# Kernel tuning notes

Hardware: AMD Instinct MI355X
Metric: run time of the kernel (lower is better)

The kernel has to match this reference:

```python
import jax, jax.numpy as jnp
import numpy as np

DECAY = 0.99
EPS = 1e-5
COMMITMENT_COST = 0.25
K = 8192   # n_embeddings
D = 256    # embedding_dim


def setup_inputs() -> dict:
    key = jax.random.key(0)
    k_z, k_w = jax.random.split(key)
    z = jax.random.normal(k_z, (16, 1024, D), dtype=jnp.float32)
    # torch init: uniform(-1/K, 1/K)
    weight = jax.random.uniform(k_w, (K, D), dtype=jnp.float32,
                                minval=-1.0 / K, maxval=1.0 / K)
    ema_cluster_size = jnp.zeros((K,), dtype=jnp.float32)
    ema_w = weight  # ema_w initialized to codebook weights
    return {"z": z, "weight": weight,
            "ema_cluster_size": ema_cluster_size, "ema_w": ema_w}


def reference(z, weight, ema_cluster_size, ema_w):
    flat = z.reshape(-1, D)                                   # [N, D]
    dist = (jnp.sum(flat * flat, axis=1, keepdims=True)
            - 2.0 * flat @ weight.T
            + jnp.sum(weight * weight, axis=1))
    idx = jnp.argmin(dist, axis=1)                            # [N]
    quantized = weight[idx].reshape(z.shape)                  # gather

    # EMA codebook update (training path)
    counts = jax.ops.segment_sum(jnp.ones_like(idx, dtype=jnp.float32),
                                 idx, num_segments=K)          # [K]
    dw = jax.ops.segment_sum(flat, idx, num_segments=K)       # [K, D]
    new_cluster_size = DECAY * ema_cluster_size + (1.0 - DECAY) * counts
    new_ema_w = DECAY * ema_w + (1.0 - DECAY) * dw
    n = jnp.sum(new_cluster_size)
    cluster_size = (new_cluster_size + EPS) / (n + K * EPS) * n
    new_weight = new_ema_w / cluster_size[:, None]

    # straight-through estimator + losses
    quantized_st = z + jax.lax.stop_gradient(quantized - z)
    codebook_loss = jnp.mean((jax.lax.stop_gradient(quantized) - z) ** 2)
    commitment_loss = jnp.mean((quantized - jax.lax.stop_gradient(z)) ** 2)
    loss = codebook_loss + COMMITMENT_COST * commitment_loss

    encoding_indices = idx.reshape(z.shape[:-1])
    return (quantized_st, loss, encoding_indices,
            new_weight, new_cluster_size, new_ema_w)
```

## Files before the change

### kernel.cpp

```cpp
#include <hip/hip_runtime.h>


#define NTOK 16384
#define KC   8192
#define DD   256

#define OFF_Q    0
#define OFF_LOSS 4194304
#define OFF_IDX  4194305
#define OFF_W    4210689
#define OFF_CS   6307841
#define OFF_EMA  6316033

#define DECAY_F  0.99f
#define OMD_F    0.01f
#define EPS_F    1e-5f
#define KEPS_F   0.08192f

typedef __attribute__((address_space(3))) unsigned int lds_u;
typedef const __attribute__((address_space(1))) unsigned int glob_u;

__global__ __launch_bounds__(256) void k_tr(const float* __restrict__ in,
                                            float* __restrict__ outT,
                                            int R, int C) {
    __shared__ float s[32][33];
    const int tx = threadIdx.x & 31, ty = threadIdx.x >> 5;
    const int c0 = blockIdx.x * 32, r0 = blockIdx.y * 32;
    #pragma unroll
    for (int i = 0; i < 4; ++i)
        s[ty + i * 8][tx] = in[(size_t)(r0 + ty + i * 8) * C + c0 + tx];
    __syncthreads();
    #pragma unroll
    for (int i = 0; i < 4; ++i)
        outT[(size_t)(c0 + ty + i * 8) * R + r0 + tx] = s[tx][ty + i * 8];
}

__global__ __launch_bounds__(256) void k_rownorm(const float* __restrict__ a,
                                                 float* __restrict__ outn) {
    const int wave = threadIdx.x >> 6, lane = threadIdx.x & 63;
    const int row  = blockIdx.x * 16 + wave * 4 + (lane >> 4);
    const int p    = lane & 15;
    const int h    = p >> 3, j = p & 7;
    const float* base = a + row * DD + h * 128 + j;
    float v = base[0];
    float r = __fmul_rn(v, v);
    #pragma unroll
    for (int t = 1; t < 16; ++t) {
        v = base[8 * t];
        r = __fadd_rn(r, __fmul_rn(v, v));
    }
    r = __fadd_rn(r, __shfl_xor(r, 1));
    r = __fadd_rn(r, __shfl_xor(r, 2));
    r = __fadd_rn(r, __shfl_xor(r, 4));
    r = __fadd_rn(r, __shfl_xor(r, 8));
    if (p == 0) outn[row] = r;
}

__global__ __launch_bounds__(256, 4) void k_argmin(
        const float* __restrict__ zT, const float* __restrict__ wT,
        const float* __restrict__ x2v, const float* __restrict__ w2v,
        float* __restrict__ vbuf, int* __restrict__ kbuf) {
    __shared__ float Zs[32][128];
    __shared__ float Ws[32][128];

    const int tid   = threadIdx.x;
    const int split = blockIdx.x & 7;
    const int rb    = blockIdx.x >> 3;
    const int n0    = rb * 128;
    const int cbase = split * 1024;
    const int tx4   = (tid & 15) * 4;
    const int ty4   = (tid >> 4) * 4;
    const int l     = tid & 63;
    const int wv    = tid >> 6;
    const int lcol  = (l & 31) * 4;
    const int lrow2 = l >> 5;

    float bestv[8];
    int   bestk[8];
    #pragma unroll
    for (int i = 0; i < 8; ++i) { bestv[i] = 1e30f; bestk[i] = 0; }

    for (int kt = 0; kt < 8; ++kt) {
        const int c0 = cbase + kt * 128;
        float acc[8][8] = {};
        for (int dt = 0; dt < 8; ++dt) {
            const int d0 = dt * 32;
            __syncthreads();
            #pragma unroll
            for (int q = 0; q < 4; ++q) {
                const int m  = wv * 4 + q;
                const int dd = m * 2 + lrow2;
                const float* gz = zT + (size_t)(d0 + dd) * NTOK + n0 + lcol;
                const float* gw = wT + (size_t)(d0 + dd) * KC   + c0 + lcol;
                __builtin_amdgcn_global_load_lds(
                    (glob_u*)gz, (lds_u*)((char*)&Zs[0][0] + m * 1024 + l * 16),
                    16, 0, 0);
                __builtin_amdgcn_global_load_lds(
                    (glob_u*)gw, (lds_u*)((char*)&Ws[0][0] + m * 1024 + l * 16),
                    16, 0, 0);
            }
            __syncthreads();
            #pragma unroll 8
            for (int dd = 0; dd < 32; ++dd) {
                const float4 a0 = *(const float4*)&Zs[dd][ty4];
                const float4 a1 = *(const float4*)&Zs[dd][64 + ty4];
                const float4 b0 = *(const float4*)&Ws[dd][tx4];
                const float4 b1 = *(const float4*)&Ws[dd][64 + tx4];
                const float av[8] = {a0.x, a0.y, a0.z, a0.w, a1.x, a1.y, a1.z, a1.w};
                const float bw[8] = {b0.x, b0.y, b0.z, b0.w, b1.x, b1.y, b1.z, b1.w};
                #pragma unroll
                for (int i = 0; i < 8; ++i)
                    #pragma unroll
                    for (int j = 0; j < 8; ++j)
                        acc[i][j] = __fmaf_rn(av[i], bw[j], acc[i][j]);
            }
        }
        #pragma unroll
        for (int j = 0; j < 8; ++j) {
            const int   code = c0 + ((j < 4) ? (tx4 + j) : (64 + tx4 + j - 4));
            const float w2   = w2v[code];
            #pragma unroll
            for (int i = 0; i < 8; ++i) {
                const int   row = n0 + ((i < 4) ? (ty4 + i) : (64 + ty4 + i - 4));
                const float x2  = x2v[row];
                const float dv  = __fadd_rn(
                    __fsub_rn(x2, __fmul_rn(2.0f, acc[i][j])), w2);
                if (dv < bestv[i] || (dv == bestv[i] && code < bestk[i])) {
                    bestv[i] = dv; bestk[i] = code;
                }
            }
        }
    }

    #pragma unroll
    for (int i = 0; i < 8; ++i) {
        float bv = bestv[i];
        int   bk = bestk[i];
        #pragma unroll
        for (int off = 8; off; off >>= 1) {
            const float ov = __shfl_down(bv, off, 16);
            const int   ok = __shfl_down(bk, off, 16);
            if (ov < bv || (ov == bv && ok < bk)) { bv = ov; bk = ok; }
        }
        if ((tid & 15) == 0) {
            const int row = n0 + ((i < 4) ? (ty4 + i) : (64 + ty4 + i - 4));
            vbuf[split * NTOK + row] = bv;
            kbuf[split * NTOK + row] = bk;
        }
    }
}

__global__ __launch_bounds__(256) void k_reduce(const float* __restrict__ vbuf,
                                                const int* __restrict__ kbuf,
                                                int* __restrict__ idx_ws,
                                                float* __restrict__ out) {
    const int r = blockIdx.x * 256 + threadIdx.x;
    float bv = vbuf[r];
    int   bk = kbuf[r];
    #pragma unroll
    for (int s = 1; s < 8; ++s) {
        const float v = vbuf[s * NTOK + r];
        const int   k = kbuf[s * NTOK + r];
        if (v < bv || (v == bv && k < bk)) { bv = v; bk = k; }
    }
    idx_ws[r] = bk;
    out[OFF_IDX + r] = (float)bk;
}

__global__ __launch_bounds__(256) void k_init(const float* __restrict__ emaw,
                                              const float* __restrict__ ecs,
                                              float* __restrict__ out,
                                              float* __restrict__ lossacc) {
    const int i = blockIdx.x * 256 + threadIdx.x;
    out[OFF_EMA + i] = __fmul_rn(DECAY_F, emaw[i]);
    if (i < KC) out[OFF_CS + i] = __fmul_rn(DECAY_F, ecs[i]);
    if (i == 0) *lossacc = 0.0f;
}

__global__ __launch_bounds__(256) void k_scatter(const float* __restrict__ z,
                                                 const float* __restrict__ w,
                                                 const int* __restrict__ idx_ws,
                                                 float* __restrict__ out,
                                                 float* __restrict__ lossacc) {
    const int n = blockIdx.x, d = threadIdx.x;
    const int k = idx_ws[n];
    const float zv   = z[n * DD + d];
    const float q    = w[k * DD + d];
    const float diff = __fsub_rn(q, zv);
    out[OFF_Q + n * DD + d] = __fadd_rn(zv, diff);

    float s = __fmul_rn(diff, diff);
    #pragma unroll
    for (int off = 32; off; off >>= 1) s += __shfl_down(s, off, 64);
    __shared__ float ps[4];
    if ((d & 63) == 0) ps[d >> 6] = s;
    __syncthreads();
    if (d == 0) atomicAdd(lossacc, ps[0] + ps[1] + ps[2] + ps[3]);

    atomicAdd(&out[OFF_EMA + k * DD + d], __fmul_rn(OMD_F, zv));
    if (d == 0) atomicAdd(&out[OFF_CS + k], OMD_F);
}

__global__ __launch_bounds__(256) void k_nsum(float* __restrict__ out,
                                              const float* __restrict__ lossacc,
                                              float* __restrict__ nsum) {
    const int t = threadIdx.x;
    float s = 0.0f;
    for (int i = t; i < KC; i += 256) s += out[OFF_CS + i];
    #pragma unroll
    for (int off = 32; off; off >>= 1) s += __shfl_down(s, off, 64);
    __shared__ float ps[4];
    if ((t & 63) == 0) ps[t >> 6] = s;
    __syncthreads();
    if (t == 0) {
        *nsum = ps[0] + ps[1] + ps[2] + ps[3];
        out[OFF_LOSS] = 1.25f * (*lossacc) / 4194304.0f;
    }
}

__global__ __launch_bounds__(256) void k_neww(float* __restrict__ out,
                                              const float* __restrict__ nsum) {
    const int k = blockIdx.x, d = threadIdx.x;
    const float n  = *nsum;
    const float cs = __fmul_rn(__fdiv_rn(__fadd_rn(out[OFF_CS + k], EPS_F),
                                         __fadd_rn(n, KEPS_F)), n);
    out[OFF_W + k * DD + d] = __fdiv_rn(out[OFF_EMA + k * DD + d], cs);
}

extern "C" void kernel_launch(void* const* d_in, const int* in_sizes, int n_in,
                              void* d_out, int out_size, void* d_ws, size_t ws_size,
                              hipStream_t stream) {
    const float* z    = (const float*)d_in[0];
    const float* w    = (const float*)d_in[1];
    const float* ecs  = (const float*)d_in[2];
    const float* emaw = (const float*)d_in[3];
    float* out = (float*)d_out;

    int*   idx_ws  = (int*)d_ws;
    float* x2v     = (float*)d_ws + NTOK;
    float* w2v     = x2v + NTOK;
    float* lossacc = w2v + KC;
    float* nsum    = lossacc + 1;

    float* zT   = out + OFF_Q;
    float* wT   = out + OFF_W;
    float* vbuf = out + OFF_EMA;
    int*   kbuf = (int*)(out + OFF_EMA) + 8 * NTOK;

    k_tr     <<<dim3(8, 512),     256, 0, stream>>>(z, zT, NTOK, DD);
    k_tr     <<<dim3(8, 256),     256, 0, stream>>>(w, wT, KC, DD);
    k_rownorm<<<NTOK / 16,        256, 0, stream>>>(z, x2v);
    k_rownorm<<<KC / 16,          256, 0, stream>>>(w, w2v);
    k_argmin <<<1024,             256, 0, stream>>>(zT, wT, x2v, w2v, vbuf, kbuf);
    k_reduce <<<NTOK / 256,       256, 0, stream>>>(vbuf, kbuf, idx_ws, out);
    k_init   <<<(KC * DD) / 256,  256, 0, stream>>>(emaw, ecs, out, lossacc);
    k_scatter<<<NTOK,             256, 0, stream>>>(z, w, idx_ws, out, lossacc);
    k_nsum   <<<1,                256, 0, stream>>>(out, lossacc, nsum);
    k_neww   <<<KC,               256, 0, stream>>>(out, nsum);
}
```

Before: 1.151 ms.

## Fuse prep kernels into one launch and stream codebook tiles from global

The two transposes, two row-norm kernels, and most of the EMA/cluster-size init are merged into one k_prep launch with a block-index dispatch. The EMA init for the region overlapping the argmin scratch buffer is deferred to a small k_init2 after the reduce. In k_argmin the codebook tile is no longer staged in LDS: each thread loads its float4 W values straight from global memory with one-step register prefetch, which halves LDS traffic and size. The cost is more global/L2 load pressure and latency exposure in the inner FMA loop.

```diff
diff --git a/kernel.cpp b/kernel.cpp
--- a/kernel.cpp
+++ b/kernel.cpp
@@ -12,6 +12,8 @@
 #define OFF_CS   6307841
 #define OFF_EMA  6316033
 
+#define SCRN     262144
+
 #define DECAY_F  0.99f
 #define OMD_F    0.01f
 #define EPS_F    1e-5f
@@ -20,25 +22,10 @@
 typedef __attribute__((address_space(3))) unsigned int lds_u;
 typedef const __attribute__((address_space(1))) unsigned int glob_u;
 
-__global__ __launch_bounds__(256) void k_tr(const float* __restrict__ in,
-                                            float* __restrict__ outT,
-                                            int R, int C) {
-    __shared__ float s[32][33];
-    const int tx = threadIdx.x & 31, ty = threadIdx.x >> 5;
-    const int c0 = blockIdx.x * 32, r0 = blockIdx.y * 32;
-    #pragma unroll
-    for (int i = 0; i < 4; ++i)
-        s[ty + i * 8][tx] = in[(size_t)(r0 + ty + i * 8) * C + c0 + tx];
-    __syncthreads();
-    #pragma unroll
-    for (int i = 0; i < 4; ++i)
-        outT[(size_t)(c0 + ty + i * 8) * R + r0 + tx] = s[tx][ty + i * 8];
-}
-
-__global__ __launch_bounds__(256) void k_rownorm(const float* __restrict__ a,
-                                                 float* __restrict__ outn) {
+__device__ __forceinline__ void rownorm_body(const float* __restrict__ a,
+                                             float* __restrict__ outn, int rb) {
     const int wave = threadIdx.x >> 6, lane = threadIdx.x & 63;
-    const int row  = blockIdx.x * 16 + wave * 4 + (lane >> 4);
+    const int row  = rb * 16 + wave * 4 + (lane >> 4);
     const int p    = lane & 15;
     const int h    = p >> 3, j = p & 7;
     const float* base = a + row * DD + h * 128 + j;
@@ -56,12 +43,51 @@
     if (p == 0) outn[row] = r;
 }
 
+__device__ __forceinline__ void tr_body(const float* __restrict__ in,
+                                        float* __restrict__ outT,
+                                        int R, int C, int b) {
+    __shared__ float s[32][33];
+    const int tx = threadIdx.x & 31, ty = threadIdx.x >> 5;
+    const int c0 = (b & 7) * 32, r0 = (b >> 3) * 32;
+    #pragma unroll
+    for (int i = 0; i < 4; ++i)
+        s[ty + i * 8][tx] = in[(size_t)(r0 + ty + i * 8) * C + c0 + tx];
+    __syncthreads();
+    #pragma unroll
+    for (int i = 0; i < 4; ++i)
+        outT[(size_t)(c0 + ty + i * 8) * R + r0 + tx] = s[tx][ty + i * 8];
+}
+
+__global__ __launch_bounds__(256) void k_prep(const float* __restrict__ z,
+                                              const float* __restrict__ w,
+                                              const float* __restrict__ ecs,
+                                              const float* __restrict__ emaw,
+                                              float* __restrict__ out,
+                                              float* __restrict__ x2v,
+                                              float* __restrict__ w2v,
+                                              float* __restrict__ lossacc) {
+    const int b = blockIdx.x;
+    if (b < 4096) {
+        tr_body(z, out + OFF_Q, NTOK, DD, b);
+    } else if (b < 6144) {
+        tr_body(w, out + OFF_W, KC, DD, b - 4096);
+    } else if (b < 7168) {
+        rownorm_body(z, x2v, b - 6144);
+    } else if (b < 7680) {
+        rownorm_body(w, w2v, b - 7168);
+    } else {
+        const int i = (b - 7680) * 256 + threadIdx.x;
+        if (i >= SCRN) out[OFF_EMA + i] = __fmul_rn(DECAY_F, emaw[i]);
+        if (i < KC) out[OFF_CS + i] = __fmul_rn(DECAY_F, ecs[i]);
+        if (i == 0) *lossacc = 0.0f;
+    }
+}
+
 __global__ __launch_bounds__(256, 4) void k_argmin(
         const float* __restrict__ zT, const float* __restrict__ wT,
         const float* __restrict__ x2v, const float* __restrict__ w2v,
         float* __restrict__ vbuf, int* __restrict__ kbuf) {
     __shared__ float Zs[32][128];
-    __shared__ float Ws[32][128];
 
     const int tid   = threadIdx.x;
     const int split = blockIdx.x & 7;
@@ -82,7 +108,12 @@
 
     for (int kt = 0; kt < 8; ++kt) {
         const int c0 = cbase + kt * 128;
+        const float* __restrict__ wc0 = wT + c0 + tx4;
+        const float* __restrict__ wc1 = wT + c0 + 64 + tx4;
         float acc[8][8] = {};
+        float4 b0 = *(const float4*)&wc0[0];
+        float4 b1 = *(const float4*)&wc1[0];
+
         for (int dt = 0; dt < 8; ++dt) {
             const int d0 = dt * 32;
             __syncthreads();
@@ -90,24 +121,23 @@
             for (int q = 0; q < 4; ++q) {
                 const int m  = wv * 4 + q;
                 const int dd = m * 2 + lrow2;
-                const float* gz = zT + (size_t)(d0 + dd) * NTOK + n0 + lcol;
-                const float* gw = wT + (size_t)(d0 + dd) * KC   + c0 + lcol;
                 __builtin_amdgcn_global_load_lds(
-                    (glob_u*)gz, (lds_u*)((char*)&Zs[0][0] + m * 1024 + l * 16),
-                    16, 0, 0);
-                __builtin_amdgcn_global_load_lds(
-                    (glob_u*)gw, (lds_u*)((char*)&Ws[0][0] + m * 1024 + l * 16),
-                    16, 0, 0);
+                    (glob_u*)(zT + (size_t)(d0 + dd) * NTOK + n0 + lcol),
+                    (lds_u*)((char*)&Zs[0][0] + m * 1024 + l * 16), 16, 0, 0);
             }
             __syncthreads();
-            #pragma unroll 8
+            #pragma unroll
             for (int dd = 0; dd < 32; ++dd) {
+                const float4 cb0 = b0, cb1 = b1;
+                const int dn = d0 + dd + 1 < DD ? d0 + dd + 1 : DD - 1;
+                b0 = *(const float4*)&wc0[(size_t)dn * KC];
+                b1 = *(const float4*)&wc1[(size_t)dn * KC];
                 const float4 a0 = *(const float4*)&Zs[dd][ty4];
                 const float4 a1 = *(const float4*)&Zs[dd][64 + ty4];
-                const float4 b0 = *(const float4*)&Ws[dd][tx4];
-                const float4 b1 = *(const float4*)&Ws[dd][64 + tx4];
-                const float av[8] = {a0.x, a0.y, a0.z, a0.w, a1.x, a1.y, a1.z, a1.w};
-                const float bw[8] = {b0.x, b0.y, b0.z, b0.w, b1.x, b1.y, b1.z, b1.w};
+                const float av[8] = {a0.x, a0.y, a0.z, a0.w,
+                                     a1.x, a1.y, a1.z, a1.w};
+                const float bw[8] = {cb0.x, cb0.y, cb0.z, cb0.w,
+                                     cb1.x, cb1.y, cb1.z, cb1.w};
                 #pragma unroll
                 for (int i = 0; i < 8; ++i)
                     #pragma unroll
@@ -167,14 +197,10 @@
     out[OFF_IDX + r] = (float)bk;
 }
 
-__global__ __launch_bounds__(256) void k_init(const float* __restrict__ emaw,
-                                              const float* __restrict__ ecs,
-                                              float* __restrict__ out,
-                                              float* __restrict__ lossacc) {
+__global__ __launch_bounds__(256) void k_init2(const float* __restrict__ emaw,
+                                               float* __restrict__ out) {
     const int i = blockIdx.x * 256 + threadIdx.x;
     out[OFF_EMA + i] = __fmul_rn(DECAY_F, emaw[i]);
-    if (i < KC) out[OFF_CS + i] = __fmul_rn(DECAY_F, ecs[i]);
-    if (i == 0) *lossacc = 0.0f;
 }
 
 __global__ __launch_bounds__(256) void k_scatter(const float* __restrict__ z,
@@ -247,14 +273,11 @@
     float* vbuf = out + OFF_EMA;
     int*   kbuf = (int*)(out + OFF_EMA) + 8 * NTOK;
 
-    k_tr     <<<dim3(8, 512),     256, 0, stream>>>(z, zT, NTOK, DD);
-    k_tr     <<<dim3(8, 256),     256, 0, stream>>>(w, wT, KC, DD);
-    k_rownorm<<<NTOK / 16,        256, 0, stream>>>(z, x2v);
-    k_rownorm<<<KC / 16,          256, 0, stream>>>(w, w2v);
-    k_argmin <<<1024,             256, 0, stream>>>(zT, wT, x2v, w2v, vbuf, kbuf);
-    k_reduce <<<NTOK / 256,       256, 0, stream>>>(vbuf, kbuf, idx_ws, out);
-    k_init   <<<(KC * DD) / 256,  256, 0, stream>>>(emaw, ecs, out, lossacc);
-    k_scatter<<<NTOK,             256, 0, stream>>>(z, w, idx_ws, out, lossacc);
-    k_nsum   <<<1,                256, 0, stream>>>(out, lossacc, nsum);
-    k_neww   <<<KC,               256, 0, stream>>>(out, nsum);
-}
+    k_prep   <<<15872, 256, 0, stream>>>(z, w, ecs, emaw, out, x2v, w2v, lossacc);
+    k_argmin <<<1024,  256, 0, stream>>>(zT, wT, x2v, w2v, vbuf, kbuf);
+    k_reduce <<<NTOK / 256, 256, 0, stream>>>(vbuf, kbuf, idx_ws, out);
+    k_init2  <<<SCRN / 256, 256, 0, stream>>>(emaw, out);
+    k_scatter<<<NTOK,  256, 0, stream>>>(z, w, idx_ws, out, lossacc);
+    k_nsum   <<<1,     256, 0, stream>>>(out, lossacc, nsum);
+    k_neww   <<<KC,    256, 0, stream>>>(out, nsum);
+}
```

Result: slower. 1.391 ms (+20.9%).
